# Performance work log

Measured on AMD Instinct MI355X. Metric: run time of the kernel, lower is better.

The kernel has to match this reference:

```python
import jax, jax.numpy as jnp
import numpy as np

N, INPUTDIM, OUTDIM, GRIDSIZE = 32768, 64, 256, 32


def setup_inputs() -> dict:
    key = jax.random.key(0)
    k1, k2 = jax.random.split(key)
    x = jax.random.normal(k1, (N, INPUTDIM), dtype=jnp.float32)
    # xavier_uniform over tensor of shape (2, outdim, inputdim, gridsize):
    # fan_in = inputdim*gridsize, fan_out = outdim*gridsize (torch treats dim0=fan_out-ish,
    # but exact init scale is irrelevant for correctness; use a matching uniform range)
    fan_in = INPUTDIM * GRIDSIZE
    fan_out = OUTDIM * GRIDSIZE
    bound = float(np.sqrt(6.0 / (fan_in + fan_out)))
    fouriercoeffs = jax.random.uniform(
        k2, (2, OUTDIM, INPUTDIM, GRIDSIZE), dtype=jnp.float32,
        minval=-bound, maxval=bound)
    bias = jnp.zeros((1, OUTDIM), dtype=jnp.float32)
    return {"x": x, "fouriercoeffs": fouriercoeffs, "bias": bias}


def reference(x, fouriercoeffs, bias):
    # gridsize_param rounds back to GRIDSIZE at init -> static.
    g = fouriercoeffs.shape[-1]
    k = jnp.arange(1, g + 1, dtype=x.dtype)  # (g,)
    # Fourier feature expansion: (N, inputdim, g)
    xk = x[:, :, None] * k[None, None, :]
    c = jnp.cos(xk)
    s = jnp.sin(xk)
    # Contract over (inputdim, gridsize) -> two GEMMs over flattened dim
    y = jnp.einsum('nig,oig->no', c, fouriercoeffs[0])
    y = y + jnp.einsum('nig,oig->no', s, fouriercoeffs[1])
    y = y + bias  # (1, outdim) broadcasts over N
    return y
```

## Files before the change

kernel.cpp:

```cpp
#include <hip/hip_runtime.h>


#define IDIM 64
#define ODIM 256
#define KDIM 4096
#define BM 64

typedef __attribute__((ext_vector_type(8))) unsigned short ushort8_t;
typedef __bf16 bf16x8 __attribute__((ext_vector_type(8)));
typedef float floatx4 __attribute__((ext_vector_type(4)));

__device__ __forceinline__ unsigned short f2bf_rne(float f) {
  unsigned int u = __float_as_uint(f);
  return (unsigned short)((u + 0x7FFFu + ((u >> 16) & 1u)) >> 16);
}

__global__ void __launch_bounds__(256) wconv(const float* __restrict__ fc,
                                             unsigned short* __restrict__ Wr) {
  int t = blockIdx.x * 256 + threadIdx.x;
  int lane = t & 63;
  int j = (t >> 6) & 7;
  int bb = t >> 9;
  int wn2 = bb & 1;
  int wk = (bb >> 1) & 1;
  int kt = bb >> 2;
  int o = wn2 * 128 + j * 16 + (lane & 15);
  int g0 = (lane >> 4) * 8;
  const float* src = fc + ((size_t)wk << 19) + o * 2048 + kt * 32 + g0;
  const float4 v0 = *(const float4*)(src);
  const float4 v1 = *(const float4*)(src + 4);
  ushort8_t r;
  r[0] = f2bf_rne(v0.x);
  r[1] = f2bf_rne(v0.y);
  r[2] = f2bf_rne(v0.z);
  r[3] = f2bf_rne(v0.w);
  r[4] = f2bf_rne(v1.x);
  r[5] = f2bf_rne(v1.y);
  r[6] = f2bf_rne(v1.z);
  r[7] = f2bf_rne(v1.w);
  *(ushort8_t*)(Wr + (size_t)t * 8) = r;
}

__global__ void __launch_bounds__(256, 2) fkan_gemm(const float* __restrict__ X,
                                                    const unsigned short* __restrict__ Wr,
                                                    const float* __restrict__ bias,
                                                    float* __restrict__ out) {
  __shared__ __align__(16) unsigned char smem[66560];
  unsigned short* const AsBase = (unsigned short*)smem;
  float* const red = (float*)smem;

  const int t = threadIdx.x;
  const int wv = t >> 6;
  const int ln = t & 63;
  const int lm = ln & 15;
  const int quad = ln >> 4;
  const int wk = wv & 1;
  const int wn2 = wv >> 1;
  const int m0 = blockIdx.x * BM;

  const int arow = t >> 2;
  const int q = t & 3;
  const float g0f = (float)(8 * q + 1);

  const int ga_c = arow * 8 + (q ^ (arow & 7));
  const int ga_s = arow * 8 + ((4 + q) ^ (arow & 7));

  const unsigned short* const bwave = Wr + (size_t)(wk * 2 + wn2) * 4096 + ln * 8;

  floatx4 acc[4][8];
#pragma unroll
  for (int a = 0; a < 4; ++a)
#pragma unroll
    for (int b = 0; b < 8; ++b)
      acc[a][b] = (floatx4){0.0f, 0.0f, 0.0f, 0.0f};

  const float* xptr = X + (size_t)(m0 + arow) * IDIM;

  auto features = [&](float xv, int buf, int j) {
    const float inv2pi = 0.15915494309189535f;
    float u = xv * inv2pi;
    float u0 = u * g0f;
    float c1 = __builtin_amdgcn_cosf(u);
    float s1 = __builtin_amdgcn_sinf(u);
    float C = __builtin_amdgcn_cosf(u0);
    float S = __builtin_amdgcn_sinf(u0);
    bf16x8 cb, sb;
    cb[0] = (__bf16)C;
    sb[0] = (__bf16)S;
#pragma unroll
    for (int jj = 1; jj < 8; ++jj) {
      float Cn = __builtin_fmaf(C, c1, -(S * s1));
      float Sn = __builtin_fmaf(S, c1, (C * s1));
      C = Cn;
      S = Sn;
      cb[jj] = (__bf16)C;
      sb[jj] = (__bf16)S;
    }
    ushort8_t* As8 = (ushort8_t*)(AsBase + buf * 16384 + j * 4096);
    As8[ga_c] = __builtin_bit_cast(ushort8_t, cb);
    As8[ga_s] = __builtin_bit_cast(ushort8_t, sb);
  };

  bf16x8 breg[8];

  auto cluster = [&](int buf, int j, int reload_kt, bool do_reload) {
    const ushort8_t* A8 = (const ushort8_t*)(AsBase + buf * 16384 + j * 4096);
    const int ch = wk * 4 + quad;
    bf16x8 af[4];
#pragma unroll
    for (int mt = 0; mt < 4; ++mt) {
      int r = mt * 16 + lm;
      af[mt] = __builtin_bit_cast(bf16x8, A8[r * 8 + (ch ^ (r & 7))]);
    }
    const unsigned short* bn = bwave + (size_t)reload_kt * 16384;
    __builtin_amdgcn_s_setprio(1);
#pragma unroll
    for (int nt = 0; nt < 8; ++nt) {
#pragma unroll
      for (int mt = 0; mt < 4; ++mt)
        acc[mt][nt] = __builtin_amdgcn_mfma_f32_16x16x32_bf16(
            af[mt], breg[nt], acc[mt][nt], 0, 0, 0);
      if (do_reload)
        breg[nt] = __builtin_bit_cast(bf16x8, *(const ushort8_t*)(bn + nt * 512));
    }
    __builtin_amdgcn_s_setprio(0);
  };

  auto ktquad = [&](int s, int cur, int nxt) {
    int k0 = 4 * s;
    float xn0 = xptr[k0 + 4];
    float xn1 = xptr[k0 + 5];
    float xn2 = xptr[k0 + 6];
    float xn3 = xptr[k0 + 7];
    cluster(cur, 0, k0 + 1, true);
    features(xn0, nxt, 0);
    cluster(cur, 1, k0 + 2, true);
    features(xn1, nxt, 1);
    cluster(cur, 2, k0 + 3, true);
    features(xn2, nxt, 2);
    cluster(cur, 3, k0 + 4, true);
    features(xn3, nxt, 3);
    __syncthreads();
  };

#pragma unroll
  for (int nt = 0; nt < 8; ++nt)
    breg[nt] = __builtin_bit_cast(bf16x8, *(const ushort8_t*)(bwave + nt * 512));
  features(xptr[0], 0, 0);
  features(xptr[1], 0, 1);
  features(xptr[2], 0, 2);
  features(xptr[3], 0, 3);
  __syncthreads();

  for (int s = 0; s < 14; s += 2) {
    ktquad(s, 0, 1);
    ktquad(s + 1, 1, 0);
  }
  ktquad(14, 0, 1);

  cluster(1, 0, 61, true);
  cluster(1, 1, 62, true);
  cluster(1, 2, 63, true);
  cluster(1, 3, 0, false);

  __syncthreads();
  if (wk == 1) {
#pragma unroll
    for (int mt = 0; mt < 4; ++mt)
#pragma unroll
      for (int nt = 0; nt < 8; ++nt) {
        int col = wn2 * 128 + nt * 16 + lm;
#pragma unroll
        for (int idx = 0; idx < 4; ++idx)
          red[(mt * 16 + quad * 4 + idx) * 260 + col] = acc[mt][nt][idx];
      }
  }
  __syncthreads();
  if (wk == 0) {
#pragma unroll
    for (int nt = 0; nt < 8; ++nt) {
      int col = wn2 * 128 + nt * 16 + lm;
      float bv = bias[col];
#pragma unroll
      for (int mt = 0; mt < 4; ++mt) {
        int rbase = m0 + mt * 16 + quad * 4;
#pragma unroll
        for (int idx = 0; idx < 4; ++idx)
          out[(size_t)(rbase + idx) * ODIM + col] =
              acc[mt][nt][idx] + red[(mt * 16 + quad * 4 + idx) * 260 + col] + bv;
      }
    }
  }
}

extern "C" void kernel_launch(void* const* d_in, const int* in_sizes, int n_in,
                              void* d_out, int out_size, void* d_ws, size_t ws_size,
                              hipStream_t stream) {
  const float* x = (const float*)d_in[0];
  const float* fc = (const float*)d_in[1];
  const float* bias = (const float*)d_in[2];
  float* out = (float*)d_out;
  unsigned short* Wr = (unsigned short*)d_ws;

  hipLaunchKernelGGL(wconv, dim3(512), dim3(256), 0, stream, fc, Wr);
  hipLaunchKernelGGL(fkan_gemm, dim3(512), dim3(256), 0, stream, x, Wr, bias, out);
}
```

Before: 128.3 us.

## Switch to 32x32x16 MFMA with N-split waves, removing split-K reduction

Replaces 16x16x32 bf16 MFMAs with 32x32x16 MFMAs and re-lays out both the weight prepack and the shared-memory feature tiles to match the new operand fragment layout. Each wave now owns a 64-column slice over the full K range, so the cross-wave split-K reduction through shared memory and its extra barriers are gone. The larger MFMA tile cuts operand fetches per FLOP, but the new unswizzled LDS layout may cause bank conflicts, and register pressure changes.

```diff
diff --git a/kernel.cpp b/kernel.cpp
--- a/kernel.cpp
+++ b/kernel.cpp
@@ -8,7 +8,7 @@
 
 typedef __attribute__((ext_vector_type(8))) unsigned short ushort8_t;
 typedef __bf16 bf16x8 __attribute__((ext_vector_type(8)));
-typedef float floatx4 __attribute__((ext_vector_type(4)));
+typedef float floatx16 __attribute__((ext_vector_type(16)));
 
 __device__ __forceinline__ unsigned short f2bf_rne(float f) {
   unsigned int u = __float_as_uint(f);
@@ -19,14 +19,15 @@
                                              unsigned short* __restrict__ Wr) {
   int t = blockIdx.x * 256 + threadIdx.x;
   int lane = t & 63;
-  int j = (t >> 6) & 7;
-  int bb = t >> 9;
-  int wn2 = bb & 1;
-  int wk = (bb >> 1) & 1;
-  int kt = bb >> 2;
-  int o = wn2 * 128 + j * 16 + (lane & 15);
-  int g0 = (lane >> 4) * 8;
-  const float* src = fc + ((size_t)wk << 19) + o * 2048 + kt * 32 + g0;
+  int bb = t >> 6;
+  int ks = bb & 3;
+  int ntile = (bb >> 2) & 7;
+  int kt = bb >> 5;
+  int chunk = 2 * ks + (lane >> 5);
+  int c = chunk >> 2;
+  int g0 = (chunk & 3) * 8;
+  int o = ntile * 32 + (lane & 31);
+  const float* src = fc + ((size_t)c << 19) + o * 2048 + kt * 32 + g0;
   const float4 v0 = *(const float4*)(src);
   const float4 v1 = *(const float4*)(src + 4);
   ushort8_t r;
@@ -45,34 +46,32 @@
                                                     const unsigned short* __restrict__ Wr,
                                                     const float* __restrict__ bias,
                                                     float* __restrict__ out) {
-  __shared__ __align__(16) unsigned char smem[66560];
-  unsigned short* const AsBase = (unsigned short*)smem;
-  float* const red = (float*)smem;
+  __shared__ __align__(16) unsigned short As[2][4][4096];
 
   const int t = threadIdx.x;
   const int wv = t >> 6;
   const int ln = t & 63;
-  const int lm = ln & 15;
-  const int quad = ln >> 4;
-  const int wk = wv & 1;
-  const int wn2 = wv >> 1;
+  const int l31 = ln & 31;
+  const int khi = ln >> 5;
+  const int wn = wv;
   const int m0 = blockIdx.x * BM;
 
   const int arow = t >> 2;
   const int q = t & 3;
   const float g0f = (float)(8 * q + 1);
 
-  const int ga_c = arow * 8 + (q ^ (arow & 7));
-  const int ga_s = arow * 8 + ((4 + q) ^ (arow & 7));
+  const int off_c = ((arow >> 5) * 4 + (q >> 1)) * 512 + ((q & 1) * 32 + (arow & 31)) * 8;
+  const int off_s = off_c + 1024;
 
-  const unsigned short* const bwave = Wr + (size_t)(wk * 2 + wn2) * 4096 + ln * 8;
+  const unsigned short* const bwave = Wr + (size_t)(wn * 8) * 512 + ln * 8;
 
-  floatx4 acc[4][8];
+  floatx16 acc[2][2];
 #pragma unroll
-  for (int a = 0; a < 4; ++a)
+  for (int a = 0; a < 2; ++a)
 #pragma unroll
-    for (int b = 0; b < 8; ++b)
-      acc[a][b] = (floatx4){0.0f, 0.0f, 0.0f, 0.0f};
+    for (int b = 0; b < 2; ++b)
+#pragma unroll
+      for (int e = 0; e < 16; ++e) acc[a][b][e] = 0.0f;
 
   const float* xptr = X + (size_t)(m0 + arow) * IDIM;
 
@@ -96,32 +95,31 @@
       cb[jj] = (__bf16)C;
       sb[jj] = (__bf16)S;
     }
-    ushort8_t* As8 = (ushort8_t*)(AsBase + buf * 16384 + j * 4096);
-    As8[ga_c] = __builtin_bit_cast(ushort8_t, cb);
-    As8[ga_s] = __builtin_bit_cast(ushort8_t, sb);
+    unsigned short* base = &As[buf][j][0];
+    *(ushort8_t*)(base + off_c) = __builtin_bit_cast(ushort8_t, cb);
+    *(ushort8_t*)(base + off_s) = __builtin_bit_cast(ushort8_t, sb);
   };
 
   bf16x8 breg[8];
 
   auto cluster = [&](int buf, int j, int reload_kt, bool do_reload) {
-    const ushort8_t* A8 = (const ushort8_t*)(AsBase + buf * 16384 + j * 4096);
-    const int ch = wk * 4 + quad;
-    bf16x8 af[4];
+    const unsigned short* Abase = &As[buf][j][0];
+    bf16x8 af[8];
 #pragma unroll
-    for (int mt = 0; mt < 4; ++mt) {
-      int r = mt * 16 + lm;
-      af[mt] = __builtin_bit_cast(bf16x8, A8[r * 8 + (ch ^ (r & 7))]);
-    }
+    for (int f = 0; f < 8; ++f)
+      af[f] = __builtin_bit_cast(bf16x8, *(const ushort8_t*)(Abase + f * 512 + ln * 8));
     const unsigned short* bn = bwave + (size_t)reload_kt * 16384;
     __builtin_amdgcn_s_setprio(1);
 #pragma unroll
-    for (int nt = 0; nt < 8; ++nt) {
-#pragma unroll
-      for (int mt = 0; mt < 4; ++mt)
-        acc[mt][nt] = __builtin_amdgcn_mfma_f32_16x16x32_bf16(
-            af[mt], breg[nt], acc[mt][nt], 0, 0, 0);
+    for (int b = 0; b < 8; ++b) {
+      const int nt = b >> 2;
+      const int ks = b & 3;
+      acc[0][nt] = __builtin_amdgcn_mfma_f32_32x32x16_bf16(
+          af[ks], breg[b], acc[0][nt], 0, 0, 0);
+      acc[1][nt] = __builtin_amdgcn_mfma_f32_32x32x16_bf16(
+          af[4 + ks], breg[b], acc[1][nt], 0, 0, 0);
       if (do_reload)
-        breg[nt] = __builtin_bit_cast(bf16x8, *(const ushort8_t*)(bn + nt * 512));
+        breg[b] = __builtin_bit_cast(bf16x8, *(const ushort8_t*)(bn + b * 512));
     }
     __builtin_amdgcn_s_setprio(0);
   };
@@ -144,8 +142,8 @@
   };
 
 #pragma unroll
-  for (int nt = 0; nt < 8; ++nt)
-    breg[nt] = __builtin_bit_cast(bf16x8, *(const ushort8_t*)(bwave + nt * 512));
+  for (int b = 0; b < 8; ++b)
+    breg[b] = __builtin_bit_cast(bf16x8, *(const ushort8_t*)(bwave + b * 512));
   features(xptr[0], 0, 0);
   features(xptr[1], 0, 1);
   features(xptr[2], 0, 2);
@@ -163,31 +161,17 @@
   cluster(1, 2, 63, true);
   cluster(1, 3, 0, false);
 
-  __syncthreads();
-  if (wk == 1) {
 #pragma unroll
-    for (int mt = 0; mt < 4; ++mt)
+  for (int nt = 0; nt < 2; ++nt) {
+    int col = wn * 64 + nt * 32 + l31;
+    float bv = bias[col];
 #pragma unroll
-      for (int nt = 0; nt < 8; ++nt) {
-        int col = wn2 * 128 + nt * 16 + lm;
+    for (int mt = 0; mt < 2; ++mt) {
+      int rbase = m0 + mt * 32 + 4 * khi;
 #pragma unroll
-        for (int idx = 0; idx < 4; ++idx)
-          red[(mt * 16 + quad * 4 + idx) * 260 + col] = acc[mt][nt][idx];
-      }
-  }
-  __syncthreads();
-  if (wk == 0) {
-#pragma unroll
-    for (int nt = 0; nt < 8; ++nt) {
-      int col = wn2 * 128 + nt * 16 + lm;
-      float bv = bias[col];
-#pragma unroll
-      for (int mt = 0; mt < 4; ++mt) {
-        int rbase = m0 + mt * 16 + quad * 4;
-#pragma unroll
-        for (int idx = 0; idx < 4; ++idx)
-          out[(size_t)(rbase + idx) * ODIM + col] =
-              acc[mt][nt][idx] + red[(mt * 16 + quad * 4 + idx) * 260 + col] + bv;
+      for (int reg = 0; reg < 16; ++reg) {
+        int row = rbase + (reg & 3) + 8 * (reg >> 2);
+        out[(size_t)row * ODIM + col] = acc[mt][nt][reg] + bv;
       }
     }
   }
```

Result: slower. 138.4 us (+7.9%).

## Split output columns across two blocks and shrink per-block LDS for occupancy

Applied to the files above, without the earlier changes.

The GEMM grid becomes 2x512, with each block computing 128 of the 256 output columns instead of all of them. The weight-relayout kernel and the B-fragment indexing change to match, and the LDS staging shrinks from four k-tiles per stage to two, so more blocks fit per CU (launch bounds go to 3). The cost is that each block now recomputes the same sin/cos features for its 64 rows, doubling the transcendental work, and syncs twice as often.

```diff
diff --git a/kernel.cpp b/kernel.cpp
--- a/kernel.cpp
+++ b/kernel.cpp
@@ -19,12 +19,12 @@
                                              unsigned short* __restrict__ Wr) {
   int t = blockIdx.x * 256 + threadIdx.x;
   int lane = t & 63;
-  int j = (t >> 6) & 7;
-  int bb = t >> 9;
-  int wn2 = bb & 1;
-  int wk = (bb >> 1) & 1;
-  int kt = bb >> 2;
-  int o = wn2 * 128 + j * 16 + (lane & 15);
+  int nt = (t >> 6) & 3;
+  int wn2 = (t >> 8) & 1;
+  int wk = (t >> 9) & 1;
+  int nh = (t >> 10) & 1;
+  int kt = t >> 11;
+  int o = nh * 128 + wn2 * 64 + nt * 16 + (lane & 15);
   int g0 = (lane >> 4) * 8;
   const float* src = fc + ((size_t)wk << 19) + o * 2048 + kt * 32 + g0;
   const float4 v0 = *(const float4*)(src);
@@ -41,11 +41,11 @@
   *(ushort8_t*)(Wr + (size_t)t * 8) = r;
 }
 
-__global__ void __launch_bounds__(256, 2) fkan_gemm(const float* __restrict__ X,
+__global__ void __launch_bounds__(256, 3) fkan_gemm(const float* __restrict__ X,
                                                     const unsigned short* __restrict__ Wr,
                                                     const float* __restrict__ bias,
                                                     float* __restrict__ out) {
-  __shared__ __align__(16) unsigned char smem[66560];
+  __shared__ __align__(16) unsigned char smem[33792];
   unsigned short* const AsBase = (unsigned short*)smem;
   float* const red = (float*)smem;
 
@@ -56,7 +56,8 @@
   const int quad = ln >> 4;
   const int wk = wv & 1;
   const int wn2 = wv >> 1;
-  const int m0 = blockIdx.x * BM;
+  const int nh = blockIdx.x;
+  const int m0 = blockIdx.y * BM;
 
   const int arow = t >> 2;
   const int q = t & 3;
@@ -65,13 +66,14 @@
   const int ga_c = arow * 8 + (q ^ (arow & 7));
   const int ga_s = arow * 8 + ((4 + q) ^ (arow & 7));
 
-  const unsigned short* const bwave = Wr + (size_t)(wk * 2 + wn2) * 4096 + ln * 8;
+  const unsigned short* const bwave =
+      Wr + ((size_t)(nh * 16 + wk * 8 + wn2 * 4) * 64 + ln) * 8;
 
-  floatx4 acc[4][8];
+  floatx4 acc[4][4];
 #pragma unroll
   for (int a = 0; a < 4; ++a)
 #pragma unroll
-    for (int b = 0; b < 8; ++b)
+    for (int b = 0; b < 4; ++b)
       acc[a][b] = (floatx4){0.0f, 0.0f, 0.0f, 0.0f};
 
   const float* xptr = X + (size_t)(m0 + arow) * IDIM;
@@ -96,15 +98,15 @@
       cb[jj] = (__bf16)C;
       sb[jj] = (__bf16)S;
     }
-    ushort8_t* As8 = (ushort8_t*)(AsBase + buf * 16384 + j * 4096);
+    ushort8_t* As8 = (ushort8_t*)(AsBase + (buf * 2 + j) * 4096);
     As8[ga_c] = __builtin_bit_cast(ushort8_t, cb);
     As8[ga_s] = __builtin_bit_cast(ushort8_t, sb);
   };
 
-  bf16x8 breg[8];
+  bf16x8 breg[4];
 
   auto cluster = [&](int buf, int j, int reload_kt, bool do_reload) {
-    const ushort8_t* A8 = (const ushort8_t*)(AsBase + buf * 16384 + j * 4096);
+    const ushort8_t* A8 = (const ushort8_t*)(AsBase + (buf * 2 + j) * 4096);
     const int ch = wk * 4 + quad;
     bf16x8 af[4];
 #pragma unroll
@@ -115,7 +117,7 @@
     const unsigned short* bn = bwave + (size_t)reload_kt * 16384;
     __builtin_amdgcn_s_setprio(1);
 #pragma unroll
-    for (int nt = 0; nt < 8; ++nt) {
+    for (int nt = 0; nt < 4; ++nt) {
 #pragma unroll
       for (int mt = 0; mt < 4; ++mt)
         acc[mt][nt] = __builtin_amdgcn_mfma_f32_16x16x32_bf16(
@@ -126,68 +128,58 @@
     __builtin_amdgcn_s_setprio(0);
   };
 
-  auto ktquad = [&](int s, int cur, int nxt) {
-    int k0 = 4 * s;
-    float xn0 = xptr[k0 + 4];
-    float xn1 = xptr[k0 + 5];
-    float xn2 = xptr[k0 + 6];
-    float xn3 = xptr[k0 + 7];
+  auto ktpair = [&](int s, int cur, int nxt) {
+    int k0 = 2 * s;
+    float xn0 = xptr[k0 + 2];
+    float xn1 = xptr[k0 + 3];
     cluster(cur, 0, k0 + 1, true);
     features(xn0, nxt, 0);
     cluster(cur, 1, k0 + 2, true);
     features(xn1, nxt, 1);
-    cluster(cur, 2, k0 + 3, true);
-    features(xn2, nxt, 2);
-    cluster(cur, 3, k0 + 4, true);
-    features(xn3, nxt, 3);
     __syncthreads();
   };
 
 #pragma unroll
-  for (int nt = 0; nt < 8; ++nt)
+  for (int nt = 0; nt < 4; ++nt)
     breg[nt] = __builtin_bit_cast(bf16x8, *(const ushort8_t*)(bwave + nt * 512));
   features(xptr[0], 0, 0);
   features(xptr[1], 0, 1);
-  features(xptr[2], 0, 2);
-  features(xptr[3], 0, 3);
   __syncthreads();
 
-  for (int s = 0; s < 14; s += 2) {
-    ktquad(s, 0, 1);
-    ktquad(s + 1, 1, 0);
+  for (int s = 0; s < 30; s += 2) {
+    ktpair(s, 0, 1);
+    ktpair(s + 1, 1, 0);
   }
-  ktquad(14, 0, 1);
+  ktpair(30, 0, 1);
 
-  cluster(1, 0, 61, true);
-  cluster(1, 1, 62, true);
-  cluster(1, 2, 63, true);
-  cluster(1, 3, 0, false);
+  cluster(1, 0, 63, true);
+  cluster(1, 1, 0, false);
 
   __syncthreads();
   if (wk == 1) {
 #pragma unroll
     for (int mt = 0; mt < 4; ++mt)
 #pragma unroll
-      for (int nt = 0; nt < 8; ++nt) {
-        int col = wn2 * 128 + nt * 16 + lm;
+      for (int nt = 0; nt < 4; ++nt) {
+        int col = wn2 * 64 + nt * 16 + lm;
 #pragma unroll
         for (int idx = 0; idx < 4; ++idx)
-          red[(mt * 16 + quad * 4 + idx) * 260 + col] = acc[mt][nt][idx];
+          red[(mt * 16 + quad * 4 + idx) * 132 + col] = acc[mt][nt][idx];
       }
   }
   __syncthreads();
   if (wk == 0) {
 #pragma unroll
-    for (int nt = 0; nt < 8; ++nt) {
-      int col = wn2 * 128 + nt * 16 + lm;
-      float bv = bias[col];
+    for (int nt = 0; nt < 4; ++nt) {
+      int col = wn2 * 64 + nt * 16 + lm;
+      float bv = bias[nh * 128 + col];
 #pragma unroll
       for (int mt = 0; mt < 4; ++mt) {
         int rbase = m0 + mt * 16 + quad * 4;
 #pragma unroll
         for (int idx = 0; idx < 4; ++idx)
-          out[(size_t)(rbase + idx) * ODIM + col] =
-              acc[mt][nt][idx] + red[(mt * 16 + quad * 4 + idx) * 260 + col] + bv;
+          out[(size_t)(rbase + idx) * ODIM + nh * 128 + col] =
+              acc[mt][nt][idx] + red[(mt * 16 + quad * 4 + idx) * 132 + col] + bv;
       }
     }
   }
@@ -203,5 +195,5 @@
   unsigned short* Wr = (unsigned short*)d_ws;
 
   hipLaunchKernelGGL(wconv, dim3(512), dim3(256), 0, stream, fc, Wr);
-  hipLaunchKernelGGL(fkan_gemm, dim3(512), dim3(256), 0, stream, x, Wr, bias, out);
+  hipLaunchKernelGGL(fkan_gemm, dim3(2, 512), dim3(256), 0, stream, x, Wr, bias, out);
 }
```

After: 139.5 us. +8.8%, slower.
